# Kernel tuning notes

Hardware: AMD Instinct MI355X
Metric: run time of the kernel (lower is better)

Reference implementation:

```python
import jax, jax.numpy as jnp
import numpy as np

B, T, N, D = 8, 512, 64, 128
PRED, HEADS, HID = 96, 8, 256
KERNELS = (17, 49)
NUM_LAYERS = 1
NUM_BLOCKS = 1
IDX_T = np.arange(64)   # lowest 64 of T//2=256 rfft modes (mode_select='low')
IDX_C = np.arange(32)   # min(modes, (N+1)//2)=32 lowest channel-frequency modes


def _mov_avg(x, k):
    # x: [B, T, N]; replicate-pad (k-1)//2 on both ends, then box filter (AvgPool1d stride 1)
    pad = (k - 1) // 2
    xp = jnp.concatenate([jnp.repeat(x[:, :1], pad, axis=1), x, jnp.repeat(x[:, -1:], pad, axis=1)], axis=1)
    c = jnp.cumsum(xp, axis=1)
    c = jnp.concatenate([jnp.zeros_like(c[:, :1]), c], axis=1)
    return (c[:, k:] - c[:, :-k]) / k


def _decomp_multi(x, dec_w, dec_b):
    # series_decomp_multi: softmax-weighted mixture of moving averages
    mm = jnp.stack([_mov_avg(x, k) for k in KERNELS], axis=-1)        # [B,T,N,K]
    w = jax.nn.softmax(x[..., None] * dec_w + dec_b, axis=-1)         # Linear(1,K) on x, softmax over K
    trend = jnp.sum(mm * w, axis=-1)
    return x - trend, trend


def _complex_attn(x, Wq, Wk, Wv, Wo):
    # x: complex64 [B, L, M, D]; multi-head attention over the M selected frequency modes.
    # Real projection weights applied to complex activations; attention weights are
    # softmax over |q k^H| / sqrt(dh); values stay complex.
    Bq, L, M, Dm = x.shape
    dh = Dm // HEADS
    q = jnp.einsum('blmd,de->blme', x, Wq).reshape(Bq, L, M, HEADS, dh)
    k = jnp.einsum('blmd,de->blme', x, Wk).reshape(Bq, L, M, HEADS, dh)
    v = jnp.einsum('blmd,de->blme', x, Wv).reshape(Bq, L, M, HEADS, dh)
    s = jnp.einsum('blmhd,blnhd->blhmn', q, jnp.conj(k))              # complex scores
    w = jax.nn.softmax(jnp.abs(s) / np.sqrt(dh), axis=-1)             # real attn weights
    o = jnp.einsum('blhmn,blnhd->blmhd', w.astype(x.dtype), v).reshape(Bq, L, M, Dm)
    return jnp.einsum('blmd,de->blme', o, Wo)


def _cem(x, Wq, Wk, Wv, Wo):
    # channel-frequency attention; x: [B, N, T, D]
    xp = jnp.transpose(x, (0, 2, 1, 3))                               # [B,T,N,D]
    xf = jnp.fft.rfft(xp, axis=2)                                     # [B,T,N//2+1,D]
    xs = xf[:, :, IDX_C, :]                                           # gather selected modes
    for _ in range(NUM_LAYERS):
        xs = _complex_attn(xs, Wq, Wk, Wv, Wo)
    yf = jnp.zeros((x.shape[0], T, N // 2 + 1, D), dtype=xf.dtype).at[:, :, IDX_C, :].set(xs)
    y = jnp.fft.irfft(yf, n=N, axis=2)
    return jnp.transpose(y, (0, 2, 1, 3))


def _tem(x, Wq, Wk, Wv, Wo):
    # temporal-frequency attention; x: [B, N, T, D]
    xf = jnp.fft.rfft(x, axis=2)                                      # [B,N,T//2+1,D]
    xs = xf[:, :, IDX_T, :]
    for _ in range(NUM_LAYERS):
        xs = _complex_attn(xs, Wq, Wk, Wv, Wo)
    yf = jnp.zeros((x.shape[0], N, T // 2 + 1, D), dtype=xf.dtype).at[:, :, IDX_T, :].set(xs)
    return jnp.fft.irfft(yf, n=T, axis=2)


def setup_inputs() -> dict:
    key = jax.random.key(0)
    ks = jax.random.split(key, 24)
    r = lambda i, shape, s: jax.random.normal(ks[i], shape, jnp.float32) * s
    K = len(KERNELS)
    return {
        'x': jax.random.normal(ks[0], (B, T, N), jnp.float32),
        'embeddings': jax.random.normal(ks[1], (1, D), jnp.float32),
        'dec_w': r(2, (K,), 1.0),
        'dec_b': jnp.zeros((K,), jnp.float32),
        'mlp_w1': r(3, (T, HID), 1.0 / np.sqrt(T)),
        'mlp_b1': jnp.zeros((HID,), jnp.float32),
        'mlp_w2': r(4, (HID, HID), 1.0 / np.sqrt(HID)),
        'mlp_b2': jnp.zeros((HID,), jnp.float32),
        'mlp_w3': r(5, (HID, PRED), 1.0 / np.sqrt(HID)),
        'mlp_b3': jnp.zeros((PRED,), jnp.float32),
        'cem_Wq': r(6, (D, D), 0.02), 'cem_Wk': r(7, (D, D), 0.02),
        'cem_Wv': r(8, (D, D), 0.02), 'cem_Wo': r(9, (D, D), 0.02),
        'tem_Wq': r(10, (D, D), 0.02), 'tem_Wk': r(11, (D, D), 0.02),
        'tem_Wv': r(12, (D, D), 0.02), 'tem_Wo': r(13, (D, D), 0.02),
        'dr_w': r(14, (D, 1), 1.0 / np.sqrt(D)),
        'dr_b': jnp.zeros((1,), jnp.float32),
        'out_w': r(15, (T, PRED), 1.0 / np.sqrt(T)),
        'out_b': jnp.zeros((PRED,), jnp.float32),
        'W_fuse': jnp.ones((2,), jnp.float32),
    }


def reference(x, embeddings, dec_w, dec_b, mlp_w1, mlp_b1, mlp_w2, mlp_b2, mlp_w3, mlp_b3,
              cem_Wq, cem_Wk, cem_Wv, cem_Wo, tem_Wq, tem_Wk, tem_Wv, tem_Wo,
              dr_w, dr_b, out_w, out_b, W_fuse):
    res, trend = _decomp_multi(x, dec_w, dec_b)
    t = jnp.transpose(trend, (0, 2, 1))                               # [B,N,T]
    h = jax.nn.relu(t @ mlp_w1 + mlp_b1)
    h = jax.nn.relu(h @ mlp_w2 + mlp_b2)
    trend_out = jnp.transpose(h @ mlp_w3 + mlp_b3, (0, 2, 1))         # [B,PRED,N]
    # tokenEmb: [B,T,N] -> [B,N,T,1] * [1,D]
    xe = jnp.transpose(res, (0, 2, 1))[..., None] * embeddings[0]      # [B,N,T,D]
    for _ in range(NUM_BLOCKS):
        xe = _cem(xe, cem_Wq, cem_Wk, cem_Wv, cem_Wo)
    for _ in range(NUM_BLOCKS):
        xe = _tem(xe, tem_Wq, tem_Wk, tem_Wv, tem_Wo)
    xr = jnp.einsum('bntd,do->bnto', xe, dr_w)[..., 0] + dr_b[0]      # dim_reduction -> [B,N,T]
    xo = jnp.transpose(jnp.einsum('bnt,tp->bnp', xr, out_w) + out_b, (0, 2, 1))  # [B,PRED,N]
    return W_fuse[0] * xo + W_fuse[1] * trend_out
```

## Files before the change

kernel.cpp:

```cpp
#include <hip/hip_runtime.h>
#include <hip/hip_bf16.h>

typedef __hip_bfloat16 bf16;
typedef float v2f __attribute__((ext_vector_type(2)));

constexpr int CB = 8;
constexpr int CT = 512;
constexpr int CN = 64;
constexpr int CD = 128;
constexpr int CP = 96;
constexpr int CH = 8;
constexpr int CDH = 16;
constexpr int CHID = 256;
constexpr int CM = 32;
constexpr int CG = 64;
constexpr float TWO_PI = 6.28318530717958647692f;

__device__ __forceinline__ float LD(const void* p, size_t i, bool f) {
  return f ? ((const float*)p)[i] : __bfloat162float(((const bf16*)p)[i]);
}
template <bool F32>
__device__ __forceinline__ float LDT(const void* p, size_t i) {
  return F32 ? ((const float*)p)[i] : __bfloat162float(((const bf16*)p)[i]);
}

__device__ __forceinline__ bool detect_f32(const void* x) {
  const unsigned int* xw = (const unsigned int*)x;
  unsigned int w = xw[threadIdx.x & 63];
  unsigned int e = (w >> 7) & 0xFF;
  unsigned long long m = __ballot(e >= 0x90 || e <= 0x60);
  return __popcll(m) > 3;
}

struct MArgs {
  const void *x, *dec_w, *dec_b, *out_w, *emb, *cWq, *cWk, *cWv, *cWo;
  const void *tWq, *tWk, *tWv, *tWo, *drw, *drb, *out_b, *wfuse;
  const void *w1, *b1, *w2, *b2, *w3, *b3;
  float *trendo, *Pbuf, *ewq, *ewk, *ewv, *wod, *owr, *owi;
  void* out;
};

template <bool F32>
__device__ void k2_body(float* sm, const MArgs& a) {
  float* xbuf = sm;
  float* rows = sm;
  float* h1 = sm + 1536;
  float* h2 = sm + 2048;
  int r0 = blockIdx.x * 2;
  int b = r0 >> 6, n0 = r0 & 63;
  int tid = threadIdx.x;
  size_t xb = (size_t)b * CT * CN + n0;
  for (int i = tid; i < CT * 2; i += 256) {
    int t = i >> 1, q = i & 1;
    xbuf[t * 3 + q] = LDT<F32>(a.x, xb + (size_t)t * CN + q);
  }
  __syncthreads();
  float trv[4];
  int q = tid & 1, tl = tid >> 1, t0 = tl * 4;
  {
    float w0 = LDT<F32>(a.dec_w, 0), w1 = LDT<F32>(a.dec_w, 1);
    float c0 = LDT<F32>(a.dec_b, 0), c1 = LDT<F32>(a.dec_b, 1);
    float s17 = 0.f, s49 = 0.f;
    #pragma unroll
    for (int o = -8; o <= 8; ++o) {
      int u = t0 + o; u = u < 0 ? 0 : (u > CT - 1 ? CT - 1 : u);
      s17 += xbuf[u * 3 + q];
    }
    #pragma unroll
    for (int o = -24; o <= 24; ++o) {
      int u = t0 + o; u = u < 0 ? 0 : (u > CT - 1 ? CT - 1 : u);
      s49 += xbuf[u * 3 + q];
    }
    #pragma unroll
    for (int k = 0; k < 4; ++k) {
      int t = t0 + k;
      if (k > 0) {
        int up8 = t + 8 > CT - 1 ? CT - 1 : t + 8;
        int dn9 = t - 9 < 0 ? 0 : t - 9;
        int up24 = t + 24 > CT - 1 ? CT - 1 : t + 24;
        int dn25 = t - 25 < 0 ? 0 : t - 25;
        s17 += xbuf[up8 * 3 + q] - xbuf[dn9 * 3 + q];
        s49 += xbuf[up24 * 3 + q] - xbuf[dn25 * 3 + q];
      }
      float m0 = s17 * (1.f / 17.f), m1 = s49 * (1.f / 49.f);
      float xv = xbuf[t * 3 + q];
      float l0 = xv * w0 + c0, l1 = xv * w1 + c1;
      float mx = fmaxf(l0, l1);
      float e0 = __expf(l0 - mx), e1 = __expf(l1 - mx);
      trv[k] = (e0 * m0 + e1 * m1) / (e0 + e1);
    }
  }
  __syncthreads();
  #pragma unroll
  for (int k = 0; k < 4; ++k) rows[q * CT + t0 + k] = trv[k];
  __syncthreads();
  int c = tid;
  float a0, a1;
  {
    float bias = LDT<F32>(a.b1, c);
    a0 = a1 = 0.f;
    #pragma unroll 16
    for (int t = 0; t < CT; ++t) {
      float w = LDT<F32>(a.w1, t * CHID + c);
      a0 = fmaf(rows[t], w, a0);
      a1 = fmaf(rows[CT + t], w, a1);
    }
    h1[c] = fmaxf(a0 + bias, 0.f);
    h1[CHID + c] = fmaxf(a1 + bias, 0.f);
  }
  __syncthreads();
  {
    float bias = LDT<F32>(a.b2, c);
    a0 = a1 = 0.f;
    #pragma unroll 16
    for (int i = 0; i < CHID; ++i) {
      float w = LDT<F32>(a.w2, i * CHID + c);
      a0 = fmaf(h1[i], w, a0);
      a1 = fmaf(h1[CHID + i], w, a1);
    }
    h2[c] = fmaxf(a0 + bias, 0.f);
    h2[CHID + c] = fmaxf(a1 + bias, 0.f);
  }
  __syncthreads();
  if (tid < 2 * CP) {
    int p = tid < CP ? tid : tid - CP;
    int qh = tid < CP ? 0 : 1;
    float bias = LDT<F32>(a.b3, p);
    a0 = 0.f;
    #pragma unroll 16
    for (int i = 0; i < CHID; ++i)
      a0 = fmaf(h2[qh * CHID + i], LDT<F32>(a.w3, i * CP + p), a0);
    a.trendo[((size_t)(b * CN + n0 + qh)) * CP + p] = a0 + bias;
  }
}

__global__ __launch_bounds__(256, 4) void kS2(MArgs a) {
  __shared__ __align__(16) float sm[4608];
  bool f32 = detect_f32(a.x);
  int blk = blockIdx.x, tid = threadIdx.x;
  if (blk < 256) {
    if (f32) k2_body<true>(sm, a);
    else     k2_body<false>(sm, a);
  } else if (blk < 1280) {
    float* xl = sm;
    float2* SL = (float2*)sm;
    float* chp = sm + 3328;
    float* rowl = sm + 3328;
    float* Rr = sm + 3584;
    float* Ri = sm + 3712;
    float* aR = sm + 3840;
    float* prod = sm + 3968;
    float* chl = sm + 4096;
    float* eml = sm + 4104;
    int bk = blk - 256;
    int b = bk >> 7, tbase = (bk & 127) * 4;
    int w = tid >> 6, lane = tid & 63;
    size_t xb = (size_t)b * CT * CN;
    for (int i = tid; i < 52 * 64; i += 256) {
      int r = i >> 6, n = i & 63;
      int u = tbase - 24 + r; u = u < 0 ? 0 : (u > CT - 1 ? CT - 1 : u);
      xl[i] = LD(a.x, xb + (size_t)u * CN + n, f32);
    }
    if (tid < 128) eml[tid] = LD(a.emb, tid, f32);
    __syncthreads();
    {
      const void* Wm = (w < 2) ? a.cWq : a.cWk;
      int d0 = (w & 1) * 64;
      float p0 = 0.f, p1 = 0.f;
      #pragma unroll 16
      for (int d = d0; d < d0 + 64; ++d) {
        float em = eml[d];
        p0 = fmaf(em, LD(Wm, (size_t)d * CD + lane, f32), p0);
        p1 = fmaf(em, LD(Wm, (size_t)d * CD + 64 + lane, f32), p1);
      }
      chp[w * 128 + lane] = p0;
      chp[w * 128 + 64 + lane] = p1;
    }
    __syncthreads();
    if (tid < 128) {
      float pq = chp[tid] + chp[128 + tid];
      float pk = chp[256 + tid] + chp[384 + tid];
      prod[tid] = pq * pk;
    }
    __syncthreads();
    if (tid < CH) {
      float s = 0;
      #pragma unroll
      for (int j = 0; j < 16; ++j) s += prod[tid * 16 + j];
      chl[tid] = fabsf(s);
    }
    {
      int Lt = 24 + w;
      float w0 = LD(a.dec_w, 0, f32), w1 = LD(a.dec_w, 1, f32);
      float c0 = LD(a.dec_b, 0, f32), c1 = LD(a.dec_b, 1, f32);
      float s17 = 0;
      #pragma unroll
      for (int o = -8; o <= 8; ++o) s17 += xl[(Lt + o) * 64 + lane];
      float s49 = 0;
      #pragma unroll
      for (int o = -24; o <= 24; ++o) s49 += xl[(Lt + o) * 64 + lane];
      float m0 = s17 * (1.f / 17.f), m1 = s49 * (1.f / 49.f);
      float xv = xl[Lt * 64 + lane];
      float l0 = xv * w0 + c0, l1 = xv * w1 + c1;
      float mx = fmaxf(l0, l1);
      float e0 = __expf(l0 - mx), e1 = __expf(l1 - mx);
      float tr = (e0 * m0 + e1 * m1) / (e0 + e1);
      rowl[w * 64 + lane] = xv - tr;
    }
    __syncthreads();
    float am, amax;
    {
      int m = lane & 31, half = lane >> 5;
      float cf, sf;
      sincosf((float)m * (TWO_PI / CN), &sf, &cf);
      float wr = (half & m & 1) ? -1.f : 1.f, wi = 0.f;
      float rr = 0.f, ri = 0.f;
      const float* rw = rowl + w * 64 + half * 32;
      #pragma unroll 8
      for (int j = 0; j < 32; ++j) {
        float xv = rw[j];
        rr = fmaf(xv, wr, rr);
        ri = fmaf(-xv, wi, ri);
        float nr = wr * cf - wi * sf; wi = wi * cf + wr * sf; wr = nr;
      }
      rr += __shfl_xor(rr, 32);
      ri += __shfl_xor(ri, 32);
      am = sqrtf(rr * rr + ri * ri);
      if (half == 0) { Rr[w * 32 + m] = rr; Ri[w * 32 + m] = ri; aR[w * 32 + m] = am; }
      amax = am;
      #pragma unroll
      for (int s2 = 1; s2 < 32; s2 <<= 1) amax = fmaxf(amax, __shfl_xor(amax, s2));
    }
    __syncthreads();
    {
      float base = 0.25f * am;
      #pragma unroll
      for (int i = 0; i < 4; ++i) {
        int pair = lane + 64 * i;
        int h = pair >> 5;
        float alpha = chl[h] * base;
        float den = 0, sr = 0, si = 0;
        for (int n2 = 0; n2 < CM; ++n2) {
          float e = __expf(alpha * (aR[w * 32 + n2] - amax));
          den += e;
          sr = fmaf(e, Rr[w * 32 + n2], sr);
          si = fmaf(e, Ri[w * 32 + n2], si);
        }
        SL[w * 256 + pair] = make_float2(sr / den, si / den);
      }
    }
    __syncthreads();
    {
      int n2 = lane, t = tbase + w;
      const float2* Sw = SL + w * 256;
      float acc[8];
      #pragma unroll
      for (int h = 0; h < CH; ++h) acc[h] = Sw[h * 32].x;
      float cd, sd;
      sincosf((float)n2 * (TWO_PI / CN), &sd, &cd);
      float px = cd, py = sd;
      for (int f = 1; f < CM; ++f) {
        #pragma unroll
        for (int h = 0; h < CH; ++h) {
          float2 s = Sw[h * 32 + f];
          acc[h] += 2.f * (s.x * px - s.y * py);
        }
        float nx = px * cd - py * sd; py = py * cd + px * sd; px = nx;
      }
      float* Pb = a.Pbuf + (((size_t)(b * CN + n2)) * CT + t) * CH;
      ((float4*)Pb)[0] = make_float4(acc[0] * (1.f / CN), acc[1] * (1.f / CN),
                                     acc[2] * (1.f / CN), acc[3] * (1.f / CN));
      ((float4*)Pb)[1] = make_float4(acc[4] * (1.f / CN), acc[5] * (1.f / CN),
                                     acc[6] * (1.f / CN), acc[7] * (1.f / CN));
    }
  } else if (blk < 1344) {
    float* ps = sm;
    int g = blk - 1280;
    int tc = tid >> 7, idx = tid & 127;
    if (idx < CP) {
      int p = idx, t0 = tc * 256;
      float s0, c0v, ss, cs;
      sincosf((float)((g * t0) & (CT - 1)) * (TWO_PI / CT), &s0, &c0v);
      sincosf((float)g * (TWO_PI / CT), &ss, &cs);
      float wr = c0v, wi = s0, ar = 0.f, ai = 0.f;
      #pragma unroll 16
      for (int t = 0; t < 256; ++t) {
        float w = LD(a.out_w, (size_t)(t0 + t) * CP + p, f32);
        ar = fmaf(w, wr, ar); ai = fmaf(w, wi, ai);
        float nr = wr * cs - wi * ss; wi = wi * cs + wr * ss; wr = nr;
      }
      ps[(tc * CP + p) * 2] = ar; ps[(tc * CP + p) * 2 + 1] = ai;
    }
    __syncthreads();
    if (tid < CP) {
      a.owr[g * CP + tid] = ps[tid * 2] + ps[(CP + tid) * 2];
      a.owi[g * CP + tid] = ps[tid * 2 + 1] + ps[(CP + tid) * 2 + 1];
    }
  } else if (blk < 1356) {
    float* eml = sm;
    float* evl = sm + 128;
    float* ewoh = sm + 160;
    int bi = blk - 1344;
    int half = tid >> 7, e = tid & 127;
    int pairIdx = bi * 2 + half;
    int which = pairIdx >> 3, h = pairIdx & 7;
    if (tid < 128) eml[tid] = LD(a.emb, tid, f32);
    __syncthreads();
    if (e < 16) {
      float acc = 0;
      #pragma unroll 8
      for (int d = 0; d < CD; ++d) acc += eml[d] * LD(a.cWv, d * CD + h * CDH + e, f32);
      evl[half * 16 + e] = acc;
    }
    __syncthreads();
    {
      float acc = 0;
      #pragma unroll
      for (int j = 0; j < CDH; ++j)
        acc += evl[half * 16 + j] * LD(a.cWo, (h * CDH + j) * CD + e, f32);
      ewoh[half * 128 + e] = acc;
    }
    __syncthreads();
    {
      const void* W = which == 0 ? a.tWq : (which == 1 ? a.tWk : a.tWv);
      float acc = 0;
      #pragma unroll 8
      for (int d = 0; d < CD; ++d) acc += ewoh[half * 128 + d] * LD(W, d * CD + e, f32);
      (which == 0 ? a.ewq : (which == 1 ? a.ewk : a.ewv))[h * CD + e] = acc;
    }
  } else {
    float* drl = sm;
    if (tid < 128) drl[tid] = LD(a.drw, tid, f32);
    __syncthreads();
    if (tid < 128) {
      float acc = 0;
      #pragma unroll 8
      for (int d = 0; d < CD; ++d) acc += LD(a.tWo, tid * CD + d, f32) * drl[d];
      a.wod[tid] = acc;
    }
  }
}

__global__ __launch_bounds__(512, 4) void kC(MArgs a) {
  __shared__ __align__(16) float sm[8128];
  float* Pl = sm;
  float* QL = sm + 4352;
  float* Cl = sm + 5376;
  float* Ul = sm + 5888;
  float2* vdL = (float2*)(sm + 5952);
  float2* zL = (float2*)(sm + 6976);
  float* zrow = sm + 8000;
  bool f32 = detect_f32(a.x);
  int blk = blockIdx.x, tid = threadIdx.x;
  int b = blk >> 6, n = blk & 63;
  const float4* src4 = (const float4*)(a.Pbuf + ((size_t)(b * CN + n)) * CT * CH);
  for (int i = tid; i < 1024; i += 512) {
    float4 v = src4[i];
    int t = i >> 1, half = i & 1;
    int k = t >> 6, u = t & 63;
    float* dst = Pl + u * 68 + half * 32 + k;
    dst[0] = v.x; dst[8] = v.y; dst[16] = v.z; dst[24] = v.w;
  }
  for (int id = tid; id < 512 + 64; id += 512) {
    if (id < 512) {
      int h = id >> 6, aa = (id >> 3) & 7, b2 = id & 7;
      float c = 0;
      #pragma unroll
      for (int j = 0; j < CDH; ++j)
        c += a.ewq[aa * CD + h * CDH + j] * a.ewk[b2 * CD + h * CDH + j];
      Cl[id] = c;
    } else {
      int r = id - 512;
      int h = r >> 3, aa = r & 7;
      float c = 0;
      #pragma unroll
      for (int j = 0; j < CDH; ++j) c += a.ewv[aa * CD + h * CDH + j] * a.wod[h * CDH + j];
      Ul[r] = c;
    }
  }
  __syncthreads();
  {
    int g = tid >> 3, h = tid & 7;
    float cs, sn;
    sincosf((float)g * (TWO_PI / CT), &sn, &cs);
    float wr = 1.f, wi = 0.f;
    float car[8] = {0, 0, 0, 0, 0, 0, 0, 0};
    float cai[8] = {0, 0, 0, 0, 0, 0, 0, 0};
    #pragma unroll 4
    for (int u = 0; u < 64; ++u) {
      const float4* pu = (const float4*)(Pl + u * 68 + h * 8);
      float4 lo = pu[0], hi = pu[1];
      car[0] = fmaf(lo.x, wr, car[0]); cai[0] = fmaf(lo.x, wi, cai[0]);
      car[1] = fmaf(lo.y, wr, car[1]); cai[1] = fmaf(lo.y, wi, cai[1]);
      car[2] = fmaf(lo.z, wr, car[2]); cai[2] = fmaf(lo.z, wi, cai[2]);
      car[3] = fmaf(lo.w, wr, car[3]); cai[3] = fmaf(lo.w, wi, cai[3]);
      car[4] = fmaf(hi.x, wr, car[4]); cai[4] = fmaf(hi.x, wi, cai[4]);
      car[5] = fmaf(hi.y, wr, car[5]); cai[5] = fmaf(hi.y, wi, cai[5]);
      car[6] = fmaf(hi.z, wr, car[6]); cai[6] = fmaf(hi.z, wi, cai[6]);
      car[7] = fmaf(hi.w, wr, car[7]); cai[7] = fmaf(hi.w, wi, cai[7]);
      float nr = wr * cs + wi * sn; wi = wi * cs - wr * sn; wr = nr;
    }
    float cs8, sn8;
    sincosf((float)(g & 7) * (TWO_PI / 8.f), &sn8, &cs8);
    float pr = 1.f, pi = 0.f, qr = 0.f, qi = 0.f;
    #pragma unroll
    for (int k = 0; k < 8; ++k) {
      qr += car[k] * pr - cai[k] * pi;
      qi += cai[k] * pr + car[k] * pi;
      float nr2 = pr * cs8 + pi * sn8; pi = pi * cs8 - pr * sn8; pr = nr2;
    }
    QL[g * 16 + h * 2] = qr;
    QL[g * 16 + h * 2 + 1] = qi;
  }
  __syncthreads();
  int h = tid >> 6, m = tid & 63;
  v2f qp[8];
  {
    const v2f* qrow = (const v2f*)(QL + m * 16);
    #pragma unroll
    for (int j = 0; j < 8; ++j) qp[j] = qrow[j];
  }
  {
    float vr = 0, vi = 0;
    #pragma unroll
    for (int aa = 0; aa < 8; ++aa) {
      float u = Ul[h * 8 + aa];
      vr = fmaf(qp[aa].x, u, vr); vi = fmaf(qp[aa].y, u, vi);
    }
    vdL[h * 64 + m] = make_float2(vr, vi);
  }
  v2f uu[8], vv[8];
  #pragma unroll
  for (int bb = 0; bb < 8; ++bb) {
    v2f acc = {0.f, 0.f};
    #pragma unroll
    for (int aa = 0; aa < 8; ++aa) acc += qp[aa] * Cl[(h * 8 + aa) * 8 + bb];
    uu[bb] = acc;
    vv[bb] = (v2f){acc.y, -acc.x};
  }
  __syncthreads();
  float mx = -1e30f, den = 0.f, zr = 0.f, zi = 0.f;
  #pragma unroll 4
  for (int g = 0; g < CG; ++g) {
    const v2f* y = (const v2f*)(QL + g * 16);
    v2f sr2 = {0.f, 0.f}, si2 = {0.f, 0.f};
    #pragma unroll
    for (int j = 0; j < 8; ++j) {
      v2f yj = y[j];
      sr2 = uu[j] * yj + sr2;
      si2 = vv[j] * yj + si2;
    }
    float sr = sr2.x + sr2.y;
    float si = si2.x + si2.y;
    float s = 0.25f * sqrtf(sr * sr + si * si);
    if (s > mx) {
      float f = __expf(mx - s);
      den *= f; zr *= f; zi *= f; mx = s;
    }
    float e = __expf(s - mx);
    float2 vd = vdL[h * 64 + g];
    den += e; zr += e * vd.x; zi += e * vd.y;
  }
  {
    float rv = 1.f / den;
    zL[h * 64 + m] = make_float2(zr * rv, zi * rv);
  }
  __syncthreads();
  if (tid < 128) {
    int g = tid >> 1, c = tid & 1;
    float acc = 0;
    #pragma unroll
    for (int hh = 0; hh < CH; ++hh) acc += c ? zL[hh * 64 + g].y : zL[hh * 64 + g].x;
    zrow[g * 2 + c] = acc;
  }
  __syncthreads();
  if (tid < CP) {
    int p = tid;
    float acc = zrow[0] * a.owr[p] - zrow[1] * a.owi[p];
    #pragma unroll 8
    for (int g = 1; g < CG; ++g)
      acc += 2.f * (zrow[g * 2] * a.owr[g * CP + p] - zrow[g * 2 + 1] * a.owi[g * CP + p]);
    float xo = acc * (1.f / CT) + LD(a.drb, 0, f32) * a.owr[p] + LD(a.out_b, p, f32);
    float val = LD(a.wfuse, 0, f32) * xo
              + LD(a.wfuse, 1, f32) * a.trendo[((size_t)(b * CN + n)) * CP + p];
    size_t oidx = ((size_t)(b * CP + p)) * CN + n;
    if (f32) ((float*)a.out)[oidx] = val;
    else ((bf16*)a.out)[oidx] = __float2bfloat16(val);
  }
}

extern "C" void kernel_launch(void* const* d_in, const int* in_sizes, int n_in,
                              void* d_out, int out_size, void* d_ws, size_t ws_size,
                              hipStream_t stream) {
  float* W = (float*)d_ws;
  MArgs a;
  a.x = d_in[0];   a.emb = d_in[1];  a.dec_w = d_in[2]; a.dec_b = d_in[3];
  a.w1 = d_in[4];  a.b1 = d_in[5];   a.w2 = d_in[6];    a.b2 = d_in[7];
  a.w3 = d_in[8];  a.b3 = d_in[9];
  a.cWq = d_in[10]; a.cWk = d_in[11]; a.cWv = d_in[12]; a.cWo = d_in[13];
  a.tWq = d_in[14]; a.tWk = d_in[15]; a.tWv = d_in[16]; a.tWo = d_in[17];
  a.drw = d_in[18]; a.drb = d_in[19]; a.out_w = d_in[20]; a.out_b = d_in[21];
  a.wfuse = d_in[22];
  a.trendo = W; W += (size_t)CB * CN * CP;
  a.Pbuf = W;   W += (size_t)CB * CN * CT * CH;
  a.ewq = W;    W += CH * CD;
  a.ewk = W;    W += CH * CD;
  a.ewv = W;    W += CH * CD;
  a.wod = W;    W += CD;
  a.owr = W;    W += CG * CP;
  a.owi = W;    W += CG * CP;
  a.out = d_out;

  kS2<<<1357, 256, 0, stream>>>(a);
  kC<<<512, 512, 0, stream>>>(a);
}
```

Baseline: 185.8 us.

## Double kC threads with split reductions and restructure kS2 softmax and inverse DFT loops

kC now launches 1024 threads per block. The temporal DFT over u and the online-softmax loop over g are each split between thread pairs, and the halves are merged with xor shuffles, including a max/rescale merge for the softmax. In kS2, the per-head softmax loop computes four heads per thread at once with exp2f and shares the loads. The inverse DFT is unrolled by two with a doubled-angle twiddle and float4 loads, and the moving-average sums reuse the 17-tap sum for the 49-tap sum. The goal is more parallelism and fewer redundant loads and exps, at the cost of extra shuffles and higher register pressure per block.

```diff
diff --git a/kernel.cpp b/kernel.cpp
--- a/kernel.cpp
+++ b/kernel.cpp
@@ -193,14 +193,21 @@
       int Lt = 24 + w;
       float w0 = LD(a.dec_w, 0, f32), w1 = LD(a.dec_w, 1, f32);
       float c0 = LD(a.dec_b, 0, f32), c1 = LD(a.dec_b, 1, f32);
-      float s17 = 0;
-      #pragma unroll
-      for (int o = -8; o <= 8; ++o) s17 += xl[(Lt + o) * 64 + lane];
-      float s49 = 0;
-      #pragma unroll
-      for (int o = -24; o <= 24; ++o) s49 += xl[(Lt + o) * 64 + lane];
+      const float* xc = xl + Lt * 64 + lane;
+      float pa = 0.f, pb = 0.f;
+      #pragma unroll
+      for (int o = -8; o <= 8; o += 2) pa += xc[o * 64];
+      #pragma unroll
+      for (int o = -7; o <= 7; o += 2) pb += xc[o * 64];
+      float s17 = pa + pb;
+      float qa = 0.f, qb = 0.f;
+      #pragma unroll
+      for (int o = 9; o <= 23; o += 2) qa += xc[o * 64] + xc[-o * 64];
+      #pragma unroll
+      for (int o = 10; o <= 24; o += 2) qb += xc[o * 64] + xc[-o * 64];
+      float s49 = s17 + qa + qb;
       float m0 = s17 * (1.f / 17.f), m1 = s49 * (1.f / 49.f);
-      float xv = xl[Lt * 64 + lane];
+      float xv = xc[0];
       float l0 = xv * w0 + c0, l1 = xv * w1 + c1;
       float mx = fmaxf(l0, l1);
       float e0 = __expf(l0 - mx), e1 = __expf(l1 - mx);
@@ -233,40 +240,52 @@
     }
     __syncthreads();
     {
-      float base = 0.25f * am;
-      #pragma unroll
-      for (int i = 0; i < 4; ++i) {
-        int pair = lane + 64 * i;
-        int h = pair >> 5;
-        float alpha = chl[h] * base;
-        float den = 0, sr = 0, si = 0;
-        for (int n2 = 0; n2 < CM; ++n2) {
-          float e = __expf(alpha * (aR[w * 32 + n2] - amax));
-          den += e;
-          sr = fmaf(e, Rr[w * 32 + n2], sr);
-          si = fmaf(e, Ri[w * 32 + n2], si);
-        }
-        SL[w * 256 + pair] = make_float2(sr / den, si / den);
-      }
-    }
-    __syncthreads();
-    {
-      int n2 = lane, t = tbase + w;
+      float base2 = 0.25f * 1.44269504f * am;
+      int hb = lane >> 5;
+      float al0 = chl[hb] * base2;
+      float al1 = chl[hb + 2] * base2;
+      float al2 = chl[hb + 4] * base2;
+      float al3 = chl[hb + 6] * base2;
+      float den0 = 0, sr0 = 0, si0 = 0, den1 = 0, sr1 = 0, si1 = 0;
+      float den2 = 0, sr2 = 0, si2 = 0, den3 = 0, sr3 = 0, si3 = 0;
+      const float* aRw = aR + w * 32;
+      const float* Rrw = Rr + w * 32;
+      const float* Riw = Ri + w * 32;
+      for (int n2 = 0; n2 < CM; ++n2) {
+        float d = aRw[n2] - amax;
+        float rrn = Rrw[n2], rin = Riw[n2];
+        float e0 = exp2f(al0 * d); den0 += e0; sr0 = fmaf(e0, rrn, sr0); si0 = fmaf(e0, rin, si0);
+        float e1 = exp2f(al1 * d); den1 += e1; sr1 = fmaf(e1, rrn, sr1); si1 = fmaf(e1, rin, si1);
+        float e2 = exp2f(al2 * d); den2 += e2; sr2 = fmaf(e2, rrn, sr2); si2 = fmaf(e2, rin, si2);
+        float e3 = exp2f(al3 * d); den3 += e3; sr3 = fmaf(e3, rrn, sr3); si3 = fmaf(e3, rin, si3);
+      }
+      float r0 = 1.f / den0, r1 = 1.f / den1, r2 = 1.f / den2, r3 = 1.f / den3;
+      SL[w * 256 + lane      ] = make_float2(sr0 * r0, si0 * r0);
+      SL[w * 256 + lane + 64 ] = make_float2(sr1 * r1, si1 * r1);
+      SL[w * 256 + lane + 128] = make_float2(sr2 * r2, si2 * r2);
+      SL[w * 256 + lane + 192] = make_float2(sr3 * r3, si3 * r3);
+    }
+    __syncthreads();
+    {
+      int n2 = lane;
       const float2* Sw = SL + w * 256;
-      float acc[8];
-      #pragma unroll
-      for (int h = 0; h < CH; ++h) acc[h] = Sw[h * 32].x;
       float cd, sd;
       sincosf((float)n2 * (TWO_PI / CN), &sd, &cd);
-      float px = cd, py = sd;
-      for (int f = 1; f < CM; ++f) {
+      float c2 = cd * cd - sd * sd, s2 = 2.f * sd * cd;
+      float pxA = 1.f, pyA = 0.f;
+      float acc[8];
+      #pragma unroll
+      for (int h = 0; h < CH; ++h) acc[h] = -Sw[h * 32].x;
+      for (int f2 = 0; f2 < 16; ++f2) {
+        float pxB = pxA * cd - pyA * sd, pyB = pyA * cd + pxA * sd;
         #pragma unroll
         for (int h = 0; h < CH; ++h) {
-          float2 s = Sw[h * 32 + f];
-          acc[h] += 2.f * (s.x * px - s.y * py);
+          float4 sv = *(const float4*)(Sw + h * 32 + f2 * 2);
+          acc[h] += 2.f * (sv.x * pxA - sv.y * pyA) + 2.f * (sv.z * pxB - sv.w * pyB);
         }
-        float nx = px * cd - py * sd; py = py * cd + px * sd; px = nx;
-      }
+        float nx = pxA * c2 - pyA * s2; pyA = pyA * c2 + pxA * s2; pxA = nx;
+      }
+      int t = tbase + w;
       float* Pb = a.Pbuf + (((size_t)(b * CN + n2)) * CT + t) * CH;
       ((float4*)Pb)[0] = make_float4(acc[0] * (1.f / CN), acc[1] * (1.f / CN),
                                      acc[2] * (1.f / CN), acc[3] * (1.f / CN));
@@ -341,7 +360,7 @@
   }
 }
 
-__global__ __launch_bounds__(512, 4) void kC(MArgs a) {
+__global__ __launch_bounds__(1024, 4) void kC(MArgs a) {
   __shared__ __align__(16) float sm[8128];
   float* Pl = sm;
   float* QL = sm + 4352;
@@ -354,23 +373,23 @@
   int blk = blockIdx.x, tid = threadIdx.x;
   int b = blk >> 6, n = blk & 63;
   const float4* src4 = (const float4*)(a.Pbuf + ((size_t)(b * CN + n)) * CT * CH);
-  for (int i = tid; i < 1024; i += 512) {
-    float4 v = src4[i];
-    int t = i >> 1, half = i & 1;
+  {
+    float4 v = src4[tid];
+    int t = tid >> 1, half = tid & 1;
     int k = t >> 6, u = t & 63;
     float* dst = Pl + u * 68 + half * 32 + k;
     dst[0] = v.x; dst[8] = v.y; dst[16] = v.z; dst[24] = v.w;
   }
-  for (int id = tid; id < 512 + 64; id += 512) {
-    if (id < 512) {
-      int h = id >> 6, aa = (id >> 3) & 7, b2 = id & 7;
+  if (tid < 576) {
+    if (tid < 512) {
+      int h = tid >> 6, aa = (tid >> 3) & 7, b2 = tid & 7;
       float c = 0;
       #pragma unroll
       for (int j = 0; j < CDH; ++j)
         c += a.ewq[aa * CD + h * CDH + j] * a.ewk[b2 * CD + h * CDH + j];
-      Cl[id] = c;
+      Cl[tid] = c;
     } else {
-      int r = id - 512;
+      int r = tid - 512;
       int h = r >> 3, aa = r & 7;
       float c = 0;
       #pragma unroll
@@ -380,15 +399,18 @@
   }
   __syncthreads();
   {
-    int g = tid >> 3, h = tid & 7;
+    int g = tid >> 4, h = (tid >> 1) & 7, uh = tid & 1;
     float cs, sn;
     sincosf((float)g * (TWO_PI / CT), &sn, &cs);
-    float wr = 1.f, wi = 0.f;
+    float s0, c0;
+    sincosf((float)(g * uh) * (TWO_PI / 16.f), &s0, &c0);
+    float wr = c0, wi = -s0;
     float car[8] = {0, 0, 0, 0, 0, 0, 0, 0};
     float cai[8] = {0, 0, 0, 0, 0, 0, 0, 0};
+    const float* Pbase = Pl + (uh * 32) * 68 + h * 8;
     #pragma unroll 4
-    for (int u = 0; u < 64; ++u) {
-      const float4* pu = (const float4*)(Pl + u * 68 + h * 8);
+    for (int u = 0; u < 32; ++u) {
+      const float4* pu = (const float4*)(Pbase + u * 68);
       float4 lo = pu[0], hi = pu[1];
       car[0] = fmaf(lo.x, wr, car[0]); cai[0] = fmaf(lo.x, wi, cai[0]);
       car[1] = fmaf(lo.y, wr, car[1]); cai[1] = fmaf(lo.y, wi, cai[1]);
@@ -400,27 +422,38 @@
       car[7] = fmaf(hi.w, wr, car[7]); cai[7] = fmaf(hi.w, wi, cai[7]);
       float nr = wr * cs + wi * sn; wi = wi * cs - wr * sn; wr = nr;
     }
-    float cs8, sn8;
-    sincosf((float)(g & 7) * (TWO_PI / 8.f), &sn8, &cs8);
-    float pr = 1.f, pi = 0.f, qr = 0.f, qi = 0.f;
     #pragma unroll
     for (int k = 0; k < 8; ++k) {
-      qr += car[k] * pr - cai[k] * pi;
-      qi += cai[k] * pr + car[k] * pi;
-      float nr2 = pr * cs8 + pi * sn8; pi = pi * cs8 - pr * sn8; pr = nr2;
-    }
-    QL[g * 16 + h * 2] = qr;
-    QL[g * 16 + h * 2 + 1] = qi;
-  }
-  __syncthreads();
-  int h = tid >> 6, m = tid & 63;
+      car[k] += __shfl_xor(car[k], 1);
+      cai[k] += __shfl_xor(cai[k], 1);
+    }
+    if (uh == 0) {
+      float cs8, sn8;
+      sincosf((float)(g & 7) * (TWO_PI / 8.f), &sn8, &cs8);
+      float pr = 1.f, pi = 0.f, qr = 0.f, qi = 0.f;
+      #pragma unroll
+      for (int k = 0; k < 8; ++k) {
+        qr += car[k] * pr - cai[k] * pi;
+        qi += cai[k] * pr + car[k] * pi;
+        float nr2 = pr * cs8 + pi * sn8; pi = pi * cs8 - pr * sn8; pr = nr2;
+      }
+      QL[g * 16 + h * 2] = qr;
+      QL[g * 16 + h * 2 + 1] = qi;
+    }
+  }
+  __syncthreads();
+  int h = tid >> 7, m = (tid >> 1) & 63, gh = tid & 1;
   v2f qp[8];
   {
-    const v2f* qrow = (const v2f*)(QL + m * 16);
-    #pragma unroll
-    for (int j = 0; j < 8; ++j) qp[j] = qrow[j];
-  }
-  {
+    const float4* q4 = (const float4*)(QL + m * 16);
+    #pragma unroll
+    for (int j = 0; j < 4; ++j) {
+      float4 qv = q4[j];
+      qp[2 * j]     = (v2f){qv.x, qv.y};
+      qp[2 * j + 1] = (v2f){qv.z, qv.w};
+    }
+  }
+  if (gh == 0) {
     float vr = 0, vi = 0;
     #pragma unroll
     for (int aa = 0; aa < 8; ++aa) {
@@ -441,14 +474,18 @@
   __syncthreads();
   float mx = -1e30f, den = 0.f, zr = 0.f, zi = 0.f;
   #pragma unroll 4
-  for (int g = 0; g < CG; ++g) {
-    const v2f* y = (const v2f*)(QL + g * 16);
+  for (int gi = 0; gi < 32; ++gi) {
+    int g = gh * 32 + gi;
+    const float4* y4 = (const float4*)(QL + g * 16);
     v2f sr2 = {0.f, 0.f}, si2 = {0.f, 0.f};
     #pragma unroll
-    for (int j = 0; j < 8; ++j) {
-      v2f yj = y[j];
-      sr2 = uu[j] * yj + sr2;
-      si2 = vv[j] * yj + si2;
+    for (int j = 0; j < 4; ++j) {
+      float4 yv = y4[j];
+      v2f ya = {yv.x, yv.y}, yb = {yv.z, yv.w};
+      sr2 = uu[2 * j] * ya + sr2;
+      si2 = vv[2 * j] * ya + si2;
+      sr2 = uu[2 * j + 1] * yb + sr2;
+      si2 = vv[2 * j + 1] * yb + si2;
     }
     float sr = sr2.x + sr2.y;
     float si = si2.x + si2.y;
@@ -462,8 +499,19 @@
     den += e; zr += e * vd.x; zi += e * vd.y;
   }
   {
-    float rv = 1.f / den;
-    zL[h * 64 + m] = make_float2(zr * rv, zi * rv);
+    float mx2 = __shfl_xor(mx, 1);
+    float den2 = __shfl_xor(den, 1);
+    float zr2 = __shfl_xor(zr, 1);
+    float zi2 = __shfl_xor(zi, 1);
+    float M = fmaxf(mx, mx2);
+    float ea = __expf(mx - M), eb = __expf(mx2 - M);
+    den = den * ea + den2 * eb;
+    zr = zr * ea + zr2 * eb;
+    zi = zi * ea + zi2 * eb;
+    if (gh == 0) {
+      float rv = 1.f / den;
+      zL[h * 64 + m] = make_float2(zr * rv, zi * rv);
+    }
   }
   __syncthreads();
   if (tid < 128) {
@@ -512,5 +560,5 @@
   a.out = d_out;
 
   kS2<<<1357, 256, 0, stream>>>(a);
-  kC<<<512, 512, 0, stream>>>(a);
-}
+  kC<<<512, 1024, 0, stream>>>(a);
+}
```

Result: slower. 189.6 us (+2.0%).
